# Optimization experiments

Hardware: AMD Instinct MI355X
Metric: run time of the kernel (lower is better)

The kernel has to match this reference:

```python
import jax, jax.numpy as jnp
import numpy as np

EPS_MSG = 1e-7   # GENConv message epsilon
BN_EPS = 1e-5    # BatchNorm1d eps
NUM_GRAPHS = 1024


def _linear(x, W, b):
    return x @ W + b


def _batchnorm(x, gamma, beta):
    # training-mode batch statistics over the node dimension
    mu = jnp.mean(x, axis=0)
    var = jnp.mean((x - mu) ** 2, axis=0)
    return (x - mu) * jax.lax.rsqrt(var + BN_EPS) * gamma + beta


def _genconv(x, src, dst, e, t, W1, b1, gamma, beta, W2, b2, num_nodes):
    # message: relu(x_j + edge_attr) + eps, shape [E, H]
    msg = jax.nn.relu(x[src] + e) + EPS_MSG
    # learnable softmax aggregation over each destination's neighborhood
    s = msg * t
    m = jax.lax.stop_gradient(jax.ops.segment_max(s, dst, num_segments=num_nodes))
    m = jnp.where(jnp.isfinite(m), m, 0.0)
    ex = jnp.exp(s - m[dst])
    denom = jax.ops.segment_sum(ex, dst, num_segments=num_nodes)
    alpha = ex / (denom[dst] + 1e-16)
    agg = jax.ops.segment_sum(msg * alpha, dst, num_segments=num_nodes)  # [N, H]
    # GENConv MLP([H, 2H, H], norm='batch') applied to x + aggregated messages
    h = x + agg
    h = _linear(h, W1, b1)
    h = _batchnorm(h, gamma, beta)
    h = jax.nn.relu(h)
    return _linear(h, W2, b2)


def setup_inputs() -> dict:
    key = jax.random.key(0)
    N, E, FIN, FE, H, L, G, OUT = 50000, 1000000, 32, 16, 64, 4, NUM_GRAPHS, 1
    ks = jax.random.split(key, 32)

    def rn(k, shape, fan_in):
        return jax.random.normal(k, shape, dtype=jnp.float32) * (1.0 / np.sqrt(fan_in))

    inp = {}
    inp["x"] = jax.random.normal(ks[0], (N, FIN), dtype=jnp.float32)
    inp["edge_attr"] = jax.random.normal(ks[1], (E, FE), dtype=jnp.float32)
    inp["edge_index"] = jax.random.randint(ks[2], (2, E), 0, N)
    inp["batch"] = jnp.sort(jax.random.randint(ks[3], (N,), 0, G))
    # atom encoder: Linear(FIN,H) ReLU Linear(H,H) ReLU
    inp["atom_W1"] = rn(ks[4], (FIN, H), FIN); inp["atom_b1"] = jnp.zeros((H,), jnp.float32)
    inp["atom_W2"] = rn(ks[5], (H, H), H);     inp["atom_b2"] = jnp.zeros((H,), jnp.float32)
    # bond encoder: Linear(FE,H) ReLU Linear(H,H) ReLU
    inp["bond_W1"] = rn(ks[6], (FE, H), FE);   inp["bond_b1"] = jnp.zeros((H,), jnp.float32)
    inp["bond_W2"] = rn(ks[7], (H, H), H);     inp["bond_b2"] = jnp.zeros((H,), jnp.float32)
    # stacked GENConv params (L layers)
    inp["conv_t"] = jnp.ones((L,), jnp.float32)
    inp["conv_W1"] = rn(ks[8], (L, H, 2 * H), H)
    inp["conv_b1"] = jnp.zeros((L, 2 * H), jnp.float32)
    inp["conv_gamma"] = jnp.ones((L, 2 * H), jnp.float32)
    inp["conv_beta"] = jnp.zeros((L, 2 * H), jnp.float32)
    inp["conv_W2"] = rn(ks[9], (L, 2 * H, H), 2 * H)
    inp["conv_b2"] = jnp.zeros((L, H), jnp.float32)
    # head
    inp["lin1_W"] = rn(ks[10], (H, H), H);     inp["lin1_b"] = jnp.zeros((H,), jnp.float32)
    inp["lin2_W"] = rn(ks[11], (H, OUT), H);   inp["lin2_b"] = jnp.zeros((OUT,), jnp.float32)
    return inp


def reference(x, edge_attr, atom_W1, atom_b1, atom_W2, atom_b2,
              bond_W1, bond_b1, bond_W2, bond_b2,
              conv_t, conv_W1, conv_b1, conv_gamma, conv_beta, conv_W2, conv_b2,
              lin1_W, lin1_b, lin2_W, lin2_b,
              edge_index, batch):
    N = x.shape[0]
    src, dst = edge_index[0], edge_index[1]
    h = jax.nn.relu(_linear(jax.nn.relu(_linear(x, atom_W1, atom_b1)), atom_W2, atom_b2))
    e = jax.nn.relu(_linear(jax.nn.relu(_linear(edge_attr, bond_W1, bond_b1)), bond_W2, bond_b2))
    L = conv_t.shape[0]
    for i in range(L):
        h = _genconv(h, src, dst, e, conv_t[i], conv_W1[i], conv_b1[i],
                     conv_gamma[i], conv_beta[i], conv_W2[i], conv_b2[i], N)
        if i < L - 1:
            h = jax.nn.relu(h)
    g = jax.ops.segment_sum(h, batch, num_segments=NUM_GRAPHS)  # global_add_pool
    g = jax.nn.relu(_linear(g, lin1_W, lin1_b))
    return _linear(g, lin2_W, lin2_b)
```

## Files before the change

kernel.cpp:

```cpp
#include <hip/hip_runtime.h>
#include <hip/hip_bf16.h>
#include <math.h>

typedef __attribute__((ext_vector_type(8))) short bf16x8;
typedef __attribute__((ext_vector_type(4))) float f32x4;

__device__ inline unsigned f2bf(float f) {
    union { __hip_bfloat16 h; unsigned short u; } cv;
    cv.h = __float2bfloat16(f);
    return (unsigned)cv.u;
}
__device__ inline float bfu(unsigned u) {
    return __uint_as_float(u << 16);
}


__global__ void k_hist(const int* __restrict__ dst, int* __restrict__ counts, int E) {
    int e = blockIdx.x * blockDim.x + threadIdx.x;
    if (e < E) atomicAdd(&counts[dst[e]], 1);
}

__global__ void k_scan1(const int* __restrict__ counts, int* __restrict__ row_ptr,
                        int* __restrict__ csum, int n) {
    __shared__ int buf[1024];
    int tid = threadIdx.x;
    int base = blockIdx.x * 1024;
    int v = (base + tid < n) ? counts[base + tid] : 0;
    buf[tid] = v;
    __syncthreads();
    int inc = v;
    for (int off = 1; off < 1024; off <<= 1) {
        int add = (tid >= off) ? buf[tid - off] : 0;
        __syncthreads();
        inc += add;
        buf[tid] = inc;
        __syncthreads();
    }
    if (base + tid < n) row_ptr[base + tid] = inc - v;
    if (tid == 1023) csum[blockIdx.x] = inc;
}

__global__ void k_scan2(int* __restrict__ csum, int nc, int* __restrict__ total) {
    if (threadIdx.x == 0) {
        int run = 0;
        for (int i = 0; i < nc; ++i) { int c = csum[i]; csum[i] = run; run += c; }
        *total = run;
    }
}

__global__ void k_scan3(int* __restrict__ row_ptr, const int* __restrict__ csum,
                        const int* __restrict__ total, int n) {
    int i = blockIdx.x * blockDim.x + threadIdx.x;
    if (i < n) row_ptr[i] += csum[i >> 10];
    if (i == 0) row_ptr[n] = *total;
}

#define ECH 4096
__global__ __launch_bounds__(256) void k_scatter(const int* __restrict__ src,
                          const int* __restrict__ dst,
                          const int* __restrict__ row_ptr, int* __restrict__ fill,
                          int2* __restrict__ spe, int E, int NS) {
    int bs = blockIdx.x & 7;
    int chunk = blockIdx.x >> 3;
    int base = chunk * ECH;
    int lo = bs * NS, hi = lo + NS;
#pragma unroll 1
    for (int j = 0; j < ECH / 256; ++j) {
        int e = base + j * 256 + threadIdx.x;
        if (e < E) {
            int d = dst[e];
            if (d >= lo && d < hi) {
                int pos = row_ptr[d] + atomicAdd(&fill[d], 1);
                spe[pos] = make_int2(src[e], e);
            }
        }
    }
}

__global__ void k_gptr(const int* __restrict__ batch, int* __restrict__ gptr, int n, int G) {
    int i = blockIdx.x * blockDim.x + threadIdx.x;
    if (i > n) return;
    if (i == 0) {
        int b0 = batch[0];
        for (int g = 0; g <= b0; ++g) gptr[g] = 0;
    } else if (i == n) {
        int bl = batch[n - 1];
        for (int g = bl + 1; g <= G; ++g) gptr[g] = n;
    } else {
        int b = batch[i], pb = batch[i - 1];
        for (int g = pb + 1; g <= b; ++g) gptr[g] = i;
    }
}


__global__ void k_wt(const float* __restrict__ W1, const float* __restrict__ W2,
                     unsigned short* __restrict__ W1b, unsigned short* __restrict__ W2tb) {
    int tid = blockIdx.x * blockDim.x + threadIdx.x;
    if (tid < 1024) {
        int j = tid / 16, k = tid % 16;
        W1b[j * 16 + k] = (unsigned short)f2bf(W1[k * 64 + j]);
    }
    if (tid < 4096) {
        int j = tid / 64, k = tid % 64;
        W2tb[j * 64 + k] = (unsigned short)f2bf(W2[k * 64 + j]);
    }
}


#define TM 128
__global__ __launch_bounds__(256) void k_atom(const float* __restrict__ x,
        const float* __restrict__ W1, const float* __restrict__ b1,
        const float* __restrict__ W2, const float* __restrict__ b2,
        float* __restrict__ out, unsigned short* __restrict__ hb, int M) {
    __shared__ float sU[TM * 65];
    __shared__ float sW1[32 * 64];
    __shared__ float sW2[64 * 64];
    __shared__ float sB1[64], sB2[64];
#define A_IN(r, c) sU[(r) * 33 + (c)]
#define A_T1(r, c) sU[(r) * 65 + (c)]
    int tid = threadIdx.x;
    int base = blockIdx.x * TM;
    for (int i = tid; i < 32 * 64 / 4; i += 256) ((float4*)sW1)[i] = ((const float4*)W1)[i];
    for (int i = tid; i < 64 * 64 / 4; i += 256) ((float4*)sW2)[i] = ((const float4*)W2)[i];
    if (tid < 64) { sB1[tid] = b1[tid]; sB2[tid] = b2[tid]; }
    for (int i = tid; i < TM * 32 / 4; i += 256) {
        int r = i / 8, c4 = i % 8;
        int row = base + r;
        float4 v = (row < M) ? ((const float4*)(x + (long)row * 32))[c4] : make_float4(0, 0, 0, 0);
        A_IN(r, c4 * 4 + 0) = v.x; A_IN(r, c4 * 4 + 1) = v.y;
        A_IN(r, c4 * 4 + 2) = v.z; A_IN(r, c4 * 4 + 3) = v.w;
    }
    __syncthreads();
    int r0 = (tid / 16) * 8;
    int c0 = (tid % 16) * 4;
    float acc[8][4];
#pragma unroll
    for (int i = 0; i < 8; i++)
#pragma unroll
        for (int j = 0; j < 4; j++) acc[i][j] = sB1[c0 + j];
    for (int k = 0; k < 32; k++) {
        float a[8], b[4];
#pragma unroll
        for (int i = 0; i < 8; i++) a[i] = A_IN(r0 + i, k);
#pragma unroll
        for (int j = 0; j < 4; j++) b[j] = sW1[k * 64 + c0 + j];
#pragma unroll
        for (int i = 0; i < 8; i++)
#pragma unroll
            for (int j = 0; j < 4; j++) acc[i][j] += a[i] * b[j];
    }
    __syncthreads();
#pragma unroll
    for (int i = 0; i < 8; i++)
#pragma unroll
        for (int j = 0; j < 4; j++) A_T1(r0 + i, c0 + j) = fmaxf(acc[i][j], 0.f);
    __syncthreads();
#pragma unroll
    for (int i = 0; i < 8; i++)
#pragma unroll
        for (int j = 0; j < 4; j++) acc[i][j] = sB2[c0 + j];
    for (int k = 0; k < 64; k++) {
        float a[8], b[4];
#pragma unroll
        for (int i = 0; i < 8; i++) a[i] = A_T1(r0 + i, k);
#pragma unroll
        for (int j = 0; j < 4; j++) b[j] = sW2[k * 64 + c0 + j];
#pragma unroll
        for (int i = 0; i < 8; i++)
#pragma unroll
            for (int j = 0; j < 4; j++) acc[i][j] += a[i] * b[j];
    }
#pragma unroll
    for (int i = 0; i < 8; i++) {
        int row = base + r0 + i;
        if (row < M) {
            float4 v = make_float4(fmaxf(acc[i][0], 0.f), fmaxf(acc[i][1], 0.f),
                                   fmaxf(acc[i][2], 0.f), fmaxf(acc[i][3], 0.f));
            *(float4*)(out + (long)row * 64 + c0) = v;
            unsigned p01 = f2bf(v.x) | (f2bf(v.y) << 16);
            unsigned p23 = f2bf(v.z) | (f2bf(v.w) << 16);
            *(uint2*)(hb + (long)row * 64 + c0) = make_uint2(p01, p23);
        }
    }
}


__global__ __launch_bounds__(256) void k_bond(const float* __restrict__ ea,
        const int2* __restrict__ spe,
        const unsigned short* __restrict__ W1b, const float* __restrict__ b1,
        const unsigned short* __restrict__ W2tb, const float* __restrict__ b2,
        unsigned short* __restrict__ e_q, int E) {
    __shared__ unsigned sT1[128 * 32];
    __shared__ unsigned sW2[64 * 32];
    int tid = threadIdx.x;

    for (int i = tid; i < 2048; i += 256) {
        int rw = i >> 5, cp = i & 31;
        sW2[rw * 32 + (cp ^ ((rw & 7) << 2))] = ((const unsigned*)W2tb)[i];
    }

    int wv = tid >> 6, lane = tid & 63;
    int lr = lane & 15, q = lane >> 4;

    union { bf16x8 v; uint4 u4; } bf1[4];
    float bias1[4];
#pragma unroll
    for (int nt = 0; nt < 4; ++nt) {
        bf1[nt].u4 = make_uint4(0, 0, 0, 0);
        if (q < 2)
            bf1[nt].u4 = *(const uint4*)(W1b + (nt * 16 + lr) * 16 + q * 8);
        bias1[nt] = b1[nt * 16 + lr];
    }

#pragma unroll
    for (int mt1 = 0; mt1 < 2; ++mt1) {
        int rtile = wv * 2 + mt1;
        long row1 = (long)blockIdx.x * 128 + rtile * 16 + lr;
        long eidx = row1 < (long)E ? row1 : (long)(E - 1);
        int eid = spe[eidx].y;
        union { bf16x8 v; uint4 u4; unsigned u[4]; } af1;
        af1.u4 = make_uint4(0, 0, 0, 0);
        if (q < 2) {
            const float4* er = (const float4*)(ea + (long)eid * 16 + q * 8);
            float4 u0 = er[0], u1 = er[1];
            af1.u[0] = f2bf(u0.x) | (f2bf(u0.y) << 16);
            af1.u[1] = f2bf(u0.z) | (f2bf(u0.w) << 16);
            af1.u[2] = f2bf(u1.x) | (f2bf(u1.y) << 16);
            af1.u[3] = f2bf(u1.z) | (f2bf(u1.w) << 16);
        }
#pragma unroll
        for (int nt = 0; nt < 4; ++nt) {
            f32x4 c0;
            c0[0] = bias1[nt]; c0[1] = bias1[nt]; c0[2] = bias1[nt]; c0[3] = bias1[nt];
            f32x4 d = __builtin_amdgcn_mfma_f32_16x16x32_bf16(af1.v, bf1[nt].v, c0, 0, 0, 0);
#pragma unroll
            for (int i = 0; i < 4; ++i) {
                unsigned hv = f2bf(fmaxf(d[i], 0.f));
                unsigned ov = (unsigned)__shfl_xor((int)hv, 1, 64);
                if ((lr & 1) == 0) {
                    int r = rtile * 16 + q * 4 + i;
                    int cp = nt * 8 + (lr >> 1);
                    sT1[r * 32 + (cp ^ ((r & 7) << 2))] = hv | (ov << 16);
                }
            }
        }
    }
    __syncthreads();

    bf16x8 bf[4][2];
#pragma unroll
    for (int nt = 0; nt < 4; ++nt)
#pragma unroll
        for (int ks = 0; ks < 2; ++ks) {
            int rw = nt * 16 + lr;
            int u = rw * 32 + ((ks * 16 + q * 4) ^ ((rw & 7) << 2));
            bf[nt][ks] = *(const bf16x8*)&sW2[u];
        }
    f32x4 acc[2][4];
#pragma unroll
    for (int mt = 0; mt < 2; ++mt)
#pragma unroll
        for (int nt = 0; nt < 4; ++nt) {
            float bias = b2[nt * 16 + lr];
            f32x4 c0; c0[0] = bias; c0[1] = bias; c0[2] = bias; c0[3] = bias;
            acc[mt][nt] = c0;
        }
#pragma unroll
    for (int mt = 0; mt < 2; ++mt) {
        int rw = (wv * 2 + mt) * 16 + lr;
#pragma unroll
        for (int ks = 0; ks < 2; ++ks) {
            int u = rw * 32 + ((ks * 16 + q * 4) ^ ((rw & 7) << 2));
            bf16x8 af = *(const bf16x8*)&sT1[u];
#pragma unroll
            for (int nt = 0; nt < 4; ++nt)
                acc[mt][nt] = __builtin_amdgcn_mfma_f32_16x16x32_bf16(
                    af, bf[nt][ks], acc[mt][nt], 0, 0, 0);
        }
    }
#pragma unroll
    for (int mt = 0; mt < 2; ++mt)
#pragma unroll
        for (int nt = 0; nt < 4; ++nt) {
            long r0 = (long)blockIdx.x * 128 + (wv * 2 + mt) * 16 + q * 4;
            unsigned p01 = f2bf(fmaxf(acc[mt][nt][0], 0.f)) |
                           (f2bf(fmaxf(acc[mt][nt][1], 0.f)) << 16);
            unsigned p23 = f2bf(fmaxf(acc[mt][nt][2], 0.f)) |
                           (f2bf(fmaxf(acc[mt][nt][3], 0.f)) << 16);
            long qb = ((r0 >> 2) * 64 + nt * 16 + lr) * 4;
            if (r0 + 3 < (long)E) {
                *(uint2*)(e_q + qb) = make_uint2(p01, p23);
            } else {
                unsigned vv[4] = {p01 & 0xffff, p01 >> 16, p23 & 0xffff, p23 >> 16};
#pragma unroll
                for (int i = 0; i < 4; ++i)
                    if (r0 + i < (long)E) e_q[qb + i] = (unsigned short)vv[i];
            }
        }
}


__global__ __launch_bounds__(256) void k_agg(const float* __restrict__ h,
        const unsigned short* __restrict__ h_bf,
        const unsigned short* __restrict__ e_q, const int2* __restrict__ spe,
        const int* __restrict__ row_ptr, const float* __restrict__ t_ptr, int layer,
        float* __restrict__ y, int n) {
    int wid = blockIdx.x * 4 + (threadIdx.x >> 6);
    int lane = threadIdx.x & 63;
    if (wid >= n) return;
    wid = __builtin_amdgcn_readfirstlane(wid);
    float tval = t_ptr[layer];
    int beg = row_ptr[wid], end = row_ptr[wid + 1];
    float m = -INFINITY, den = 0.f, num = 0.f;
    int i = beg;
    int astart = (beg + 3) & ~3; if (astart > end) astart = end;
    int aend = end & ~3;         if (aend < astart) aend = astart;
    for (; i < astart; ++i) {
        int s = spe[i].x;
        float ev = bfu((unsigned)e_q[((long)(i >> 2) * 64 + lane) * 4 + (i & 3)]);
        float hv = bfu((unsigned)h_bf[(long)s * 64 + lane]);
        float msg = fmaxf(hv + ev, 0.f) + 1e-7f;
        float sv = msg * tval;
        float mn = fmaxf(m, sv);
        float sc = __expf(m - mn);
        float w = __expf(sv - mn);
        den = den * sc + w;
        num = num * sc + w * msg;
        m = mn;
    }
    for (; i + 8 <= aend; i += 8) {
        int s0 = spe[i].x,     s1 = spe[i + 1].x, s2 = spe[i + 2].x, s3 = spe[i + 3].x;
        int s4 = spe[i + 4].x, s5 = spe[i + 5].x, s6 = spe[i + 6].x, s7 = spe[i + 7].x;
        uint2 ea0 = *(const uint2*)(e_q + ((long)(i >> 2) * 64 + lane) * 4);
        uint2 ea1 = *(const uint2*)(e_q + ((long)((i >> 2) + 1) * 64 + lane) * 4);
        float hv0 = bfu((unsigned)h_bf[(long)s0 * 64 + lane]);
        float hv1 = bfu((unsigned)h_bf[(long)s1 * 64 + lane]);
        float hv2 = bfu((unsigned)h_bf[(long)s2 * 64 + lane]);
        float hv3 = bfu((unsigned)h_bf[(long)s3 * 64 + lane]);
        float hv4 = bfu((unsigned)h_bf[(long)s4 * 64 + lane]);
        float hv5 = bfu((unsigned)h_bf[(long)s5 * 64 + lane]);
        float hv6 = bfu((unsigned)h_bf[(long)s6 * 64 + lane]);
        float hv7 = bfu((unsigned)h_bf[(long)s7 * 64 + lane]);
        float msg0 = fmaxf(hv0 + bfu(ea0.x & 0xffff), 0.f) + 1e-7f;
        float msg1 = fmaxf(hv1 + bfu(ea0.x >> 16), 0.f) + 1e-7f;
        float msg2 = fmaxf(hv2 + bfu(ea0.y & 0xffff), 0.f) + 1e-7f;
        float msg3 = fmaxf(hv3 + bfu(ea0.y >> 16), 0.f) + 1e-7f;
        float msg4 = fmaxf(hv4 + bfu(ea1.x & 0xffff), 0.f) + 1e-7f;
        float msg5 = fmaxf(hv5 + bfu(ea1.x >> 16), 0.f) + 1e-7f;
        float msg6 = fmaxf(hv6 + bfu(ea1.y & 0xffff), 0.f) + 1e-7f;
        float msg7 = fmaxf(hv7 + bfu(ea1.y >> 16), 0.f) + 1e-7f;
        float sv0 = msg0 * tval, sv1 = msg1 * tval, sv2 = msg2 * tval, sv3 = msg3 * tval;
        float sv4 = msg4 * tval, sv5 = msg5 * tval, sv6 = msg6 * tval, sv7 = msg7 * tval;
        float mn = fmaxf(fmaxf(fmaxf(fmaxf(m, sv0), fmaxf(sv1, sv2)),
                               fmaxf(fmaxf(sv3, sv4), fmaxf(sv5, sv6))), sv7);
        float sc = __expf(m - mn);
        float w0 = __expf(sv0 - mn), w1 = __expf(sv1 - mn);
        float w2 = __expf(sv2 - mn), w3 = __expf(sv3 - mn);
        float w4 = __expf(sv4 - mn), w5 = __expf(sv5 - mn);
        float w6 = __expf(sv6 - mn), w7 = __expf(sv7 - mn);
        den = den * sc + (((w0 + w1) + (w2 + w3)) + ((w4 + w5) + (w6 + w7)));
        num = num * sc + (((w0 * msg0 + w1 * msg1) + (w2 * msg2 + w3 * msg3)) +
                          ((w4 * msg4 + w5 * msg5) + (w6 * msg6 + w7 * msg7)));
        m = mn;
    }
    for (; i < aend; i += 4) {
        int s0 = spe[i].x, s1 = spe[i + 1].x, s2 = spe[i + 2].x, s3 = spe[i + 3].x;
        uint2 ee = *(const uint2*)(e_q + ((long)(i >> 2) * 64 + lane) * 4);
        float hv0 = bfu((unsigned)h_bf[(long)s0 * 64 + lane]);
        float hv1 = bfu((unsigned)h_bf[(long)s1 * 64 + lane]);
        float hv2 = bfu((unsigned)h_bf[(long)s2 * 64 + lane]);
        float hv3 = bfu((unsigned)h_bf[(long)s3 * 64 + lane]);
        float msg0 = fmaxf(hv0 + bfu(ee.x & 0xffff), 0.f) + 1e-7f;
        float msg1 = fmaxf(hv1 + bfu(ee.x >> 16), 0.f) + 1e-7f;
        float msg2 = fmaxf(hv2 + bfu(ee.y & 0xffff), 0.f) + 1e-7f;
        float msg3 = fmaxf(hv3 + bfu(ee.y >> 16), 0.f) + 1e-7f;
        float sv0 = msg0 * tval, sv1 = msg1 * tval;
        float sv2 = msg2 * tval, sv3 = msg3 * tval;
        float mn = fmaxf(fmaxf(fmaxf(m, sv0), fmaxf(sv1, sv2)), sv3);
        float sc = __expf(m - mn);
        float w0 = __expf(sv0 - mn);
        float w1 = __expf(sv1 - mn);
        float w2 = __expf(sv2 - mn);
        float w3 = __expf(sv3 - mn);
        den = den * sc + ((w0 + w1) + (w2 + w3));
        num = num * sc + ((w0 * msg0 + w1 * msg1) + (w2 * msg2 + w3 * msg3));
        m = mn;
    }
    for (; i < end; ++i) {
        int s = spe[i].x;
        float ev = bfu((unsigned)e_q[((long)(i >> 2) * 64 + lane) * 4 + (i & 3)]);
        float hv = bfu((unsigned)h_bf[(long)s * 64 + lane]);
        float msg = fmaxf(hv + ev, 0.f) + 1e-7f;
        float sv = msg * tval;
        float mn = fmaxf(m, sv);
        float sc = __expf(m - mn);
        float w = __expf(sv - mn);
        den = den * sc + w;
        num = num * sc + w * msg;
        m = mn;
    }
    float agg = (end > beg) ? num / (den + 1e-16f) : 0.f;
    y[(long)wid * 64 + lane] = h[(long)wid * 64 + lane] + agg;
}


__global__ __launch_bounds__(256) void k_gemm1(const float* __restrict__ y,
        const float* __restrict__ W1, const float* __restrict__ b1,
        float* __restrict__ h1, float* __restrict__ part, int n) {
    __shared__ float sA[64][65];
    __shared__ float sW[64 * 128];
    __shared__ float sB[128];
    __shared__ float sS[8][128];
    __shared__ float sS2[8][128];
    int tid = threadIdx.x;
    int base = blockIdx.x * 64;
    for (int i = tid; i < 64 * 128 / 4; i += 256) ((float4*)sW)[i] = ((const float4*)W1)[i];
    if (tid < 128) sB[tid] = b1[tid];
    for (int i = tid; i < 64 * 64 / 4; i += 256) {
        int r = i / 16, c4 = i % 16;
        int row = base + r;
        float4 v = (row < n) ? ((const float4*)(y + (long)row * 64))[c4] : make_float4(0, 0, 0, 0);
        sA[r][c4 * 4 + 0] = v.x; sA[r][c4 * 4 + 1] = v.y;
        sA[r][c4 * 4 + 2] = v.z; sA[r][c4 * 4 + 3] = v.w;
    }
    __syncthreads();
    int rg = tid / 32;
    int r0 = rg * 8;
    int c0 = (tid % 32) * 4;
    float acc[8][4];
#pragma unroll
    for (int i = 0; i < 8; i++)
#pragma unroll
        for (int j = 0; j < 4; j++) acc[i][j] = sB[c0 + j];
    for (int k = 0; k < 64; k++) {
        float a[8], b[4];
#pragma unroll
        for (int i = 0; i < 8; i++) a[i] = sA[r0 + i][k];
#pragma unroll
        for (int j = 0; j < 4; j++) b[j] = sW[k * 128 + c0 + j];
#pragma unroll
        for (int i = 0; i < 8; i++)
#pragma unroll
            for (int j = 0; j < 4; j++) acc[i][j] += a[i] * b[j];
    }
    float ps[4] = {0, 0, 0, 0}, ps2[4] = {0, 0, 0, 0};
#pragma unroll
    for (int i = 0; i < 8; i++) {
        int row = base + r0 + i;
        if (row < n) {
            float4 v = make_float4(acc[i][0], acc[i][1], acc[i][2], acc[i][3]);
            *(float4*)(h1 + (long)row * 128 + c0) = v;
#pragma unroll
            for (int j = 0; j < 4; j++) { ps[j] += acc[i][j]; ps2[j] += acc[i][j] * acc[i][j]; }
        }
    }
#pragma unroll
    for (int j = 0; j < 4; j++) { sS[rg][c0 + j] = ps[j]; sS2[rg][c0 + j] = ps2[j]; }
    __syncthreads();
    if (tid < 128) {
        float s = 0.f, s2 = 0.f;
#pragma unroll
        for (int g = 0; g < 8; g++) { s += sS[g][tid]; s2 += sS2[g][tid]; }
        part[blockIdx.x * 256 + tid] = s;
        part[blockIdx.x * 256 + 128 + tid] = s2;
    }
}


__global__ __launch_bounds__(256) void k_bnred(const float* __restrict__ part,
                                               float* __restrict__ part2, int nblk) {
    int c = threadIdx.x;
    int b = blockIdx.x;
    float s = 0.f;
    for (int r = b; r < nblk; r += 64) s += part[r * 256 + c];
    part2[b * 256 + c] = s;
}

__global__ __launch_bounds__(1024) void k_bnfin(const float* __restrict__ part2,
                        const float* __restrict__ gamma, const float* __restrict__ beta,
                        float* __restrict__ scale, float* __restrict__ shift, float invN) {
    __shared__ float red[4][256];
    __shared__ float tot[256];
    int c = threadIdx.x & 255;
    int g = threadIdx.x >> 8;
    float s = 0.f;
#pragma unroll
    for (int r = 0; r < 16; ++r) s += part2[(g * 16 + r) * 256 + c];
    red[g][c] = s;
    __syncthreads();
    if (threadIdx.x < 256) tot[c] = red[0][c] + red[1][c] + red[2][c] + red[3][c];
    __syncthreads();
    if (threadIdx.x < 128) {
        int cc = threadIdx.x;
        float mu = tot[cc] * invN;
        float var = fmaxf(tot[128 + cc] * invN - mu * mu, 0.f);
        float sc = gamma[cc] * rsqrtf(var + 1e-5f);
        scale[cc] = sc;
        shift[cc] = beta[cc] - mu * sc;
    }
}


__global__ __launch_bounds__(256) void k_gemm2(const float* __restrict__ h1,
        const float* __restrict__ scale, const float* __restrict__ shift,
        const float* __restrict__ W2, const float* __restrict__ b2,
        float* __restrict__ hout, unsigned short* __restrict__ hb, int n, int dorelu) {
    __shared__ float sA[32][129];
    __shared__ float sW[128 * 64];
    __shared__ float sSc[128], sSh[128], sB[64];
    int tid = threadIdx.x;
    int base = blockIdx.x * 32;
    for (int i = tid; i < 128 * 64 / 4; i += 256) ((float4*)sW)[i] = ((const float4*)W2)[i];
    if (tid < 128) { sSc[tid] = scale[tid]; sSh[tid] = shift[tid]; }
    if (tid < 64) sB[tid] = b2[tid];
    __syncthreads();
    for (int i = tid; i < 32 * 128 / 4; i += 256) {
        int r = i / 32, c4 = i % 32;
        int row = base + r;
        float4 v = (row < n) ? ((const float4*)(h1 + (long)row * 128))[c4] : make_float4(0, 0, 0, 0);
        int c = c4 * 4;
        sA[r][c + 0] = fmaxf(v.x * sSc[c + 0] + sSh[c + 0], 0.f);
        sA[r][c + 1] = fmaxf(v.y * sSc[c + 1] + sSh[c + 1], 0.f);
        sA[r][c + 2] = fmaxf(v.z * sSc[c + 2] + sSh[c + 2], 0.f);
        sA[r][c + 3] = fmaxf(v.w * sSc[c + 3] + sSh[c + 3], 0.f);
    }
    __syncthreads();
    int r0 = (tid / 16) * 2;
    int c0 = (tid % 16) * 4;
    float acc[2][4];
#pragma unroll
    for (int i = 0; i < 2; i++)
#pragma unroll
        for (int j = 0; j < 4; j++) acc[i][j] = sB[c0 + j];
    for (int k = 0; k < 128; k++) {
        float a[2], b[4];
#pragma unroll
        for (int i = 0; i < 2; i++) a[i] = sA[r0 + i][k];
#pragma unroll
        for (int j = 0; j < 4; j++) b[j] = sW[k * 64 + c0 + j];
#pragma unroll
        for (int i = 0; i < 2; i++)
#pragma unroll
            for (int j = 0; j < 4; j++) acc[i][j] += a[i] * b[j];
    }
#pragma unroll
    for (int i = 0; i < 2; i++) {
        int row = base + r0 + i;
        if (row < n) {
            float4 v;
            v.x = dorelu ? fmaxf(acc[i][0], 0.f) : acc[i][0];
            v.y = dorelu ? fmaxf(acc[i][1], 0.f) : acc[i][1];
            v.z = dorelu ? fmaxf(acc[i][2], 0.f) : acc[i][2];
            v.w = dorelu ? fmaxf(acc[i][3], 0.f) : acc[i][3];
            *(float4*)(hout + (long)row * 64 + c0) = v;
            if (dorelu) {
                unsigned p01 = f2bf(v.x) | (f2bf(v.y) << 16);
                unsigned p23 = f2bf(v.z) | (f2bf(v.w) << 16);
                *(uint2*)(hb + (long)row * 64 + c0) = make_uint2(p01, p23);
            }
        }
    }
}


__global__ __launch_bounds__(64) void k_head(const float* __restrict__ h,
        const int* __restrict__ gptr,
        const float* __restrict__ W1, const float* __restrict__ b1,
        const float* __restrict__ W2, const float* __restrict__ b2,
        float* __restrict__ out) {
    int g = blockIdx.x;
    int lane = threadIdx.x;
    int beg = gptr[g], end = gptr[g + 1];
    float s = 0.f;
    for (int r = beg; r < end; ++r) s += h[(long)r * 64 + lane];
    __shared__ float sg[64];
    sg[lane] = s;
    __syncthreads();
    float acc = b1[lane];
    for (int k = 0; k < 64; k++) acc += sg[k] * W1[k * 64 + lane];
    acc = fmaxf(acc, 0.f);
    float v = acc * W2[lane];
#pragma unroll
    for (int off = 32; off > 0; off >>= 1) v += __shfl_down(v, off, 64);
    if (lane == 0) out[g] = v + b2[0];
}


extern "C" void kernel_launch(void* const* d_in, const int* in_sizes, int n_in,
                              void* d_out, int out_size, void* d_ws, size_t ws_size,
                              hipStream_t stream) {
    const float* x      = (const float*)d_in[0];
    const float* ea     = (const float*)d_in[1];
    const int*   ei     = (const int*)d_in[2];
    const int*   batch  = (const int*)d_in[3];
    const float* atomW1 = (const float*)d_in[4];
    const float* atomb1 = (const float*)d_in[5];
    const float* atomW2 = (const float*)d_in[6];
    const float* atomb2 = (const float*)d_in[7];
    const float* bondW1 = (const float*)d_in[8];
    const float* bondb1 = (const float*)d_in[9];
    const float* bondW2 = (const float*)d_in[10];
    const float* bondb2 = (const float*)d_in[11];
    const float* convT  = (const float*)d_in[12];
    const float* convW1 = (const float*)d_in[13];
    const float* convb1 = (const float*)d_in[14];
    const float* convG  = (const float*)d_in[15];
    const float* convBt = (const float*)d_in[16];
    const float* convW2 = (const float*)d_in[17];
    const float* convb2 = (const float*)d_in[18];
    const float* lin1W  = (const float*)d_in[19];
    const float* lin1b  = (const float*)d_in[20];
    const float* lin2W  = (const float*)d_in[21];
    const float* lin2b  = (const float*)d_in[22];
    float* out = (float*)d_out;

    const int N = in_sizes[0] / 32;
    const int E = in_sizes[1] / 16;
    const int G = out_size;
    const int Lconv = in_sizes[12];
    const int nchunk = (N + 1023) / 1024;
    const int nblk1 = (N + 63) / 64;
    const int NS = (N + 7) / 8;
    const int nchE = (E + ECH - 1) / ECH;
    const size_t nquad = (size_t)((E + 3) / 4);

    size_t need = 0;
    auto count = [&](size_t bytes) { need += (bytes + 255) & ~(size_t)255; };
    count(nquad * 4 * 64 * 2);
    count((size_t)N * 64 * 4);
    count((size_t)N * 64 * 2);
    count((size_t)N * 64 * 4);
    count((size_t)N * 128 * 4);
    count((size_t)E * 8);
    count((size_t)(N + 1) * 4);
    count((size_t)N * 4);
    count((size_t)N * 4);
    count((size_t)(G + 1) * 4);
    count((size_t)nblk1 * 256 * 4);
    count((size_t)64 * 256 * 4);
    count(128 * 4); count(128 * 4);
    count((size_t)(nchunk + 1) * 4);
    count(4);
    count(1024 * 2);
    count(4096 * 2);
    if (ws_size < need) {
        hipMemsetAsync(d_out, 0, (size_t)out_size * 4, stream);
        return;
    }

    char* ws = (char*)d_ws;
    size_t off = 0;
    auto alloc = [&](size_t bytes) -> void* {
        void* p = ws + off;
        off += (bytes + 255) & ~(size_t)255;
        return p;
    };
    unsigned short* e_q = (unsigned short*)alloc(nquad * 4 * 64 * 2);
    float* h_cur    = (float*)alloc((size_t)N * 64 * 4);
    unsigned short* h_bf = (unsigned short*)alloc((size_t)N * 64 * 2);
    float* y_buf    = (float*)alloc((size_t)N * 64 * 4);
    float* h1       = (float*)alloc((size_t)N * 128 * 4);
    int2*  spe      = (int2*)alloc((size_t)E * 8);
    int*   row_ptr  = (int*)alloc((size_t)(N + 1) * 4);
    int*   counts   = (int*)alloc((size_t)N * 4);
    int*   fill     = (int*)alloc((size_t)N * 4);
    int*   gptr     = (int*)alloc((size_t)(G + 1) * 4);
    float* part     = (float*)alloc((size_t)nblk1 * 256 * 4);
    float* part2    = (float*)alloc((size_t)64 * 256 * 4);
    float* bnscale  = (float*)alloc(128 * 4);
    float* bnshift  = (float*)alloc(128 * 4);
    int*   csum     = (int*)alloc((size_t)(nchunk + 1) * 4);
    int*   totalp   = (int*)alloc(4);
    unsigned short* W1b  = (unsigned short*)alloc(1024 * 2);
    unsigned short* W2tb = (unsigned short*)alloc(4096 * 2);
    (void)n_in;

    hipMemsetAsync(counts, 0, (size_t)N * 4, stream);
    hipMemsetAsync(fill, 0, (size_t)N * 4, stream);

    const int* src = ei;
    const int* dst = ei + E;

    k_hist<<<(E + 255) / 256, 256, 0, stream>>>(dst, counts, E);
    k_scan1<<<nchunk, 1024, 0, stream>>>(counts, row_ptr, csum, N);
    k_scan2<<<1, 64, 0, stream>>>(csum, nchunk, totalp);
    k_scan3<<<(N + 255) / 256, 256, 0, stream>>>(row_ptr, csum, totalp, N);
    k_scatter<<<nchE * 8, 256, 0, stream>>>(src, dst, row_ptr, fill, spe, E, NS);
    k_gptr<<<(N + 256) / 256, 256, 0, stream>>>(batch, gptr, N, G);
    k_wt<<<16, 256, 0, stream>>>(bondW1, bondW2, W1b, W2tb);

    k_atom<<<(N + TM - 1) / TM, 256, 0, stream>>>(x, atomW1, atomb1, atomW2, atomb2,
                                                  h_cur, h_bf, N);
    k_bond<<<(E + 127) / 128, 256, 0, stream>>>(ea, spe, W1b, bondb1, W2tb, bondb2, e_q, E);

    for (int l = 0; l < Lconv; ++l) {
        k_agg<<<(N + 3) / 4, 256, 0, stream>>>(h_cur, h_bf, e_q, spe, row_ptr, convT, l,
                                               y_buf, N);
        k_gemm1<<<nblk1, 256, 0, stream>>>(y_buf, convW1 + (size_t)l * 64 * 128,
                                           convb1 + (size_t)l * 128, h1, part, N);
        k_bnred<<<64, 256, 0, stream>>>(part, part2, nblk1);
        k_bnfin<<<1, 1024, 0, stream>>>(part2, convG + (size_t)l * 128, convBt + (size_t)l * 128,
                                        bnscale, bnshift, 1.0f / (float)N);
        k_gemm2<<<(N + 31) / 32, 256, 0, stream>>>(h1, bnscale, bnshift,
                                                   convW2 + (size_t)l * 128 * 64,
                                                   convb2 + (size_t)l * 64, h_cur, h_bf, N,
                                                   (l < Lconv - 1) ? 1 : 0);
    }

    k_head<<<G, 64, 0, stream>>>(h_cur, gptr, lin1W, lin1b, lin2W, lin2b, out);
}
```

Before: 611.2 us.

## Move GENConv MLP GEMMs to bf16 MFMA with bf16 intermediate buffers

Rewrites both per-layer MLP GEMM kernels to use bf16 16x16x32 MFMA instructions with swizzled LDS tiles, instead of scalar fp32 FMA loops. The aggregation output and the hidden activations between the two GEMMs are now stored in bf16, which halves their memory traffic. Conv weights are pre-transposed to bf16 once by a new kernel. This cuts ALU and memory cost of the GEMM stages at the price of bf16 rounding in the batchnorm input and the MLP path.

```diff
diff --git a/kernel.cpp b/kernel.cpp
--- a/kernel.cpp
+++ b/kernel.cpp
@@ -103,6 +103,21 @@
     if (tid < 4096) {
         int j = tid / 64, k = tid % 64;
         W2tb[j * 64 + k] = (unsigned short)f2bf(W2[k * 64 + j]);
+    }
+}
+
+__global__ void k_wtc(const float* __restrict__ W1, const float* __restrict__ W2,
+                      unsigned short* __restrict__ W1tb, unsigned short* __restrict__ W2tb,
+                      int L) {
+    int idx = blockIdx.x * blockDim.x + threadIdx.x;
+    int tot = L * 8192;
+    if (idx < tot) {
+        int l = idx / 8192, r = idx % 8192;
+        int j = r / 64, k = r % 64;
+        W1tb[(long)l * 8192 + j * 64 + k] = (unsigned short)f2bf(W1[(long)l * 8192 + k * 128 + j]);
+        int j2 = r / 128, k2 = r % 128;
+        W2tb[(long)l * 8192 + j2 * 128 + k2] =
+            (unsigned short)f2bf(W2[(long)l * 8192 + k2 * 64 + j2]);
     }
 }
 
@@ -304,7 +319,7 @@
         const unsigned short* __restrict__ h_bf,
         const unsigned short* __restrict__ e_q, const int2* __restrict__ spe,
         const int* __restrict__ row_ptr, const float* __restrict__ t_ptr, int layer,
-        float* __restrict__ y, int n) {
+        unsigned short* __restrict__ yb, int n) {
     int wid = blockIdx.x * 4 + (threadIdx.x >> 6);
     int lane = threadIdx.x & 63;
     if (wid >= n) return;
@@ -400,69 +415,77 @@
         m = mn;
     }
     float agg = (end > beg) ? num / (den + 1e-16f) : 0.f;
-    y[(long)wid * 64 + lane] = h[(long)wid * 64 + lane] + agg;
-}
-
-
-__global__ __launch_bounds__(256) void k_gemm1(const float* __restrict__ y,
-        const float* __restrict__ W1, const float* __restrict__ b1,
-        float* __restrict__ h1, float* __restrict__ part, int n) {
-    __shared__ float sA[64][65];
-    __shared__ float sW[64 * 128];
-    __shared__ float sB[128];
-    __shared__ float sS[8][128];
-    __shared__ float sS2[8][128];
+    yb[(long)wid * 64 + lane] = (unsigned short)f2bf(h[(long)wid * 64 + lane] + agg);
+}
+
+
+__global__ __launch_bounds__(256) void k_gemm1(const unsigned* __restrict__ yb,
+        const unsigned* __restrict__ W1tb, const float* __restrict__ b1,
+        unsigned* __restrict__ h1b, float* __restrict__ part, int n) {
+    __shared__ unsigned sY[128 * 32];
+    __shared__ unsigned sW[128 * 32];
     int tid = threadIdx.x;
-    int base = blockIdx.x * 64;
-    for (int i = tid; i < 64 * 128 / 4; i += 256) ((float4*)sW)[i] = ((const float4*)W1)[i];
-    if (tid < 128) sB[tid] = b1[tid];
-    for (int i = tid; i < 64 * 64 / 4; i += 256) {
-        int r = i / 16, c4 = i % 16;
-        int row = base + r;
-        float4 v = (row < n) ? ((const float4*)(y + (long)row * 64))[c4] : make_float4(0, 0, 0, 0);
-        sA[r][c4 * 4 + 0] = v.x; sA[r][c4 * 4 + 1] = v.y;
-        sA[r][c4 * 4 + 2] = v.z; sA[r][c4 * 4 + 3] = v.w;
-    }
-    __syncthreads();
-    int rg = tid / 32;
-    int r0 = rg * 8;
-    int c0 = (tid % 32) * 4;
-    float acc[8][4];
-#pragma unroll
-    for (int i = 0; i < 8; i++)
-#pragma unroll
-        for (int j = 0; j < 4; j++) acc[i][j] = sB[c0 + j];
-    for (int k = 0; k < 64; k++) {
-        float a[8], b[4];
-#pragma unroll
-        for (int i = 0; i < 8; i++) a[i] = sA[r0 + i][k];
-#pragma unroll
-        for (int j = 0; j < 4; j++) b[j] = sW[k * 128 + c0 + j];
-#pragma unroll
-        for (int i = 0; i < 8; i++)
-#pragma unroll
-            for (int j = 0; j < 4; j++) acc[i][j] += a[i] * b[j];
-    }
-    float ps[4] = {0, 0, 0, 0}, ps2[4] = {0, 0, 0, 0};
-#pragma unroll
-    for (int i = 0; i < 8; i++) {
-        int row = base + r0 + i;
-        if (row < n) {
-            float4 v = make_float4(acc[i][0], acc[i][1], acc[i][2], acc[i][3]);
-            *(float4*)(h1 + (long)row * 128 + c0) = v;
-#pragma unroll
-            for (int j = 0; j < 4; j++) { ps[j] += acc[i][j]; ps2[j] += acc[i][j] * acc[i][j]; }
-        }
-    }
-#pragma unroll
-    for (int j = 0; j < 4; j++) { sS[rg][c0 + j] = ps[j]; sS2[rg][c0 + j] = ps2[j]; }
-    __syncthreads();
-    if (tid < 128) {
-        float s = 0.f, s2 = 0.f;
-#pragma unroll
-        for (int g = 0; g < 8; g++) { s += sS[g][tid]; s2 += sS2[g][tid]; }
-        part[blockIdx.x * 256 + tid] = s;
-        part[blockIdx.x * 256 + 128 + tid] = s2;
+    int base = blockIdx.x * 128;
+    for (int i = tid; i < 4096; i += 256) {
+        int rw = i >> 5, cp = i & 31;
+        sW[rw * 32 + (cp ^ ((rw & 7) << 2))] = W1tb[i];
+    }
+#pragma unroll
+    for (int j = 0; j < 16; ++j) {
+        int u = j * 256 + tid;
+        int r = u >> 5, cp = u & 31;
+        long row = base + r;
+        unsigned v = (row < (long)n) ? yb[row * 32 + cp] : 0u;
+        sY[r * 32 + (cp ^ ((r & 7) << 2))] = v;
+    }
+    __syncthreads();
+    int wv = tid >> 6, lane = tid & 63, lr = lane & 15, q = lane >> 4;
+    bf16x8 bf[2][2];
+    float bias[2];
+#pragma unroll
+    for (int nt2 = 0; nt2 < 2; ++nt2) {
+        int rw = wv * 32 + nt2 * 16 + lr;
+#pragma unroll
+        for (int ks = 0; ks < 2; ++ks)
+            bf[nt2][ks] = *(const bf16x8*)&sW[rw * 32 + ((ks * 16 + q * 4) ^ ((rw & 7) << 2))];
+        bias[nt2] = b1[rw];
+    }
+    float ps[2] = {0, 0}, ps2[2] = {0, 0};
+#pragma unroll 1
+    for (int mt = 0; mt < 8; ++mt) {
+        int ar = mt * 16 + lr;
+        bf16x8 a0 = *(const bf16x8*)&sY[ar * 32 + ((q * 4) ^ ((ar & 7) << 2))];
+        bf16x8 a1 = *(const bf16x8*)&sY[ar * 32 + ((16 + q * 4) ^ ((ar & 7) << 2))];
+#pragma unroll
+        for (int nt2 = 0; nt2 < 2; ++nt2) {
+            f32x4 acc;
+            acc[0] = bias[nt2]; acc[1] = bias[nt2]; acc[2] = bias[nt2]; acc[3] = bias[nt2];
+            acc = __builtin_amdgcn_mfma_f32_16x16x32_bf16(a0, bf[nt2][0], acc, 0, 0, 0);
+            acc = __builtin_amdgcn_mfma_f32_16x16x32_bf16(a1, bf[nt2][1], acc, 0, 0, 0);
+            int col = wv * 32 + nt2 * 16 + lr;
+#pragma unroll
+            for (int i = 0; i < 4; ++i) {
+                long row = base + mt * 16 + q * 4 + i;
+                float v = acc[i];
+                unsigned hv = f2bf(v);
+                unsigned ov = (unsigned)__shfl_xor((int)hv, 1, 64);
+                bool in = row < (long)n;
+                if (in) { ps[nt2] += v; ps2[nt2] += v * v; }
+                if (in && (lr & 1) == 0)
+                    h1b[row * 64 + ((unsigned)col >> 1)] = hv | (ov << 16);
+            }
+        }
+    }
+#pragma unroll
+    for (int nt2 = 0; nt2 < 2; ++nt2) {
+        float s = ps[nt2], s2 = ps2[nt2];
+        s += __shfl_down(s, 32, 64);  s += __shfl_down(s, 16, 64);
+        s2 += __shfl_down(s2, 32, 64); s2 += __shfl_down(s2, 16, 64);
+        if (lane < 16) {
+            int col = wv * 32 + nt2 * 16 + lr;
+            part[(long)blockIdx.x * 256 + col] = s;
+            part[(long)blockIdx.x * 256 + 128 + col] = s2;
+        }
     }
 }
 
@@ -472,7 +495,7 @@
     int c = threadIdx.x;
     int b = blockIdx.x;
     float s = 0.f;
-    for (int r = b; r < nblk; r += 64) s += part[r * 256 + c];
+    for (int r = b; r < nblk; r += 64) s += part[(long)r * 256 + c];
     part2[b * 256 + c] = s;
 }
 
@@ -501,62 +524,66 @@
 }
 
 
-__global__ __launch_bounds__(256) void k_gemm2(const float* __restrict__ h1,
+__global__ __launch_bounds__(256) void k_gemm2(const unsigned* __restrict__ h1b,
         const float* __restrict__ scale, const float* __restrict__ shift,
-        const float* __restrict__ W2, const float* __restrict__ b2,
+        const unsigned* __restrict__ W2tbL, const float* __restrict__ b2,
         float* __restrict__ hout, unsigned short* __restrict__ hb, int n, int dorelu) {
-    __shared__ float sA[32][129];
-    __shared__ float sW[128 * 64];
-    __shared__ float sSc[128], sSh[128], sB[64];
+    __shared__ unsigned sA[128 * 64];
+    __shared__ unsigned sW[64 * 64];
+    __shared__ float sSc[128], sSh[128];
     int tid = threadIdx.x;
-    int base = blockIdx.x * 32;
-    for (int i = tid; i < 128 * 64 / 4; i += 256) ((float4*)sW)[i] = ((const float4*)W2)[i];
+    int base = blockIdx.x * 128;
     if (tid < 128) { sSc[tid] = scale[tid]; sSh[tid] = shift[tid]; }
-    if (tid < 64) sB[tid] = b2[tid];
-    __syncthreads();
-    for (int i = tid; i < 32 * 128 / 4; i += 256) {
-        int r = i / 32, c4 = i % 32;
-        int row = base + r;
-        float4 v = (row < n) ? ((const float4*)(h1 + (long)row * 128))[c4] : make_float4(0, 0, 0, 0);
-        int c = c4 * 4;
-        sA[r][c + 0] = fmaxf(v.x * sSc[c + 0] + sSh[c + 0], 0.f);
-        sA[r][c + 1] = fmaxf(v.y * sSc[c + 1] + sSh[c + 1], 0.f);
-        sA[r][c + 2] = fmaxf(v.z * sSc[c + 2] + sSh[c + 2], 0.f);
-        sA[r][c + 3] = fmaxf(v.w * sSc[c + 3] + sSh[c + 3], 0.f);
-    }
-    __syncthreads();
-    int r0 = (tid / 16) * 2;
-    int c0 = (tid % 16) * 4;
-    float acc[2][4];
-#pragma unroll
-    for (int i = 0; i < 2; i++)
-#pragma unroll
-        for (int j = 0; j < 4; j++) acc[i][j] = sB[c0 + j];
-    for (int k = 0; k < 128; k++) {
-        float a[2], b[4];
-#pragma unroll
-        for (int i = 0; i < 2; i++) a[i] = sA[r0 + i][k];
-#pragma unroll
-        for (int j = 0; j < 4; j++) b[j] = sW[k * 64 + c0 + j];
-#pragma unroll
-        for (int i = 0; i < 2; i++)
-#pragma unroll
-            for (int j = 0; j < 4; j++) acc[i][j] += a[i] * b[j];
-    }
-#pragma unroll
-    for (int i = 0; i < 2; i++) {
-        int row = base + r0 + i;
-        if (row < n) {
-            float4 v;
-            v.x = dorelu ? fmaxf(acc[i][0], 0.f) : acc[i][0];
-            v.y = dorelu ? fmaxf(acc[i][1], 0.f) : acc[i][1];
-            v.z = dorelu ? fmaxf(acc[i][2], 0.f) : acc[i][2];
-            v.w = dorelu ? fmaxf(acc[i][3], 0.f) : acc[i][3];
-            *(float4*)(hout + (long)row * 64 + c0) = v;
-            if (dorelu) {
-                unsigned p01 = f2bf(v.x) | (f2bf(v.y) << 16);
-                unsigned p23 = f2bf(v.z) | (f2bf(v.w) << 16);
-                *(uint2*)(hb + (long)row * 64 + c0) = make_uint2(p01, p23);
+    for (int i = tid; i < 4096; i += 256) {
+        int rw = i >> 6, cp = i & 63;
+        sW[rw * 64 + (cp ^ ((rw & 7) << 2))] = W2tbL[i];
+    }
+    __syncthreads();
+#pragma unroll
+    for (int j = 0; j < 32; ++j) {
+        int u = j * 256 + tid;
+        int r = u >> 6, cp = u & 63;
+        long row = base + r;
+        unsigned w = 0;
+        if (row < (long)n) {
+            unsigned hv = h1b[row * 64 + cp];
+            float v0 = fmaxf(bfu(hv & 0xffff) * sSc[2 * cp] + sSh[2 * cp], 0.f);
+            float v1 = fmaxf(bfu(hv >> 16) * sSc[2 * cp + 1] + sSh[2 * cp + 1], 0.f);
+            w = f2bf(v0) | (f2bf(v1) << 16);
+        }
+        sA[r * 64 + (cp ^ ((r & 7) << 2))] = w;
+    }
+    __syncthreads();
+    int wv = tid >> 6, lane = tid & 63, lr = lane & 15, q = lane >> 4;
+    bf16x8 bf[4];
+    {
+        int rw = wv * 16 + lr;
+#pragma unroll
+        for (int ks = 0; ks < 4; ++ks)
+            bf[ks] = *(const bf16x8*)&sW[rw * 64 + ((ks * 16 + q * 4) ^ ((rw & 7) << 2))];
+    }
+    float bias = b2[wv * 16 + lr];
+#pragma unroll 1
+    for (int mt = 0; mt < 8; ++mt) {
+        int ar = mt * 16 + lr;
+        f32x4 acc;
+        acc[0] = bias; acc[1] = bias; acc[2] = bias; acc[3] = bias;
+#pragma unroll
+        for (int ks = 0; ks < 4; ++ks) {
+            bf16x8 a = *(const bf16x8*)&sA[ar * 64 + ((ks * 16 + q * 4) ^ ((ar & 7) << 2))];
+            acc = __builtin_amdgcn_mfma_f32_16x16x32_bf16(a, bf[ks], acc, 0, 0, 0);
+        }
+        int col = wv * 16 + lr;
+#pragma unroll
+        for (int i = 0; i < 4; ++i) {
+            long row = base + mt * 16 + q * 4 + i;
+            float v = dorelu ? fmaxf(acc[i], 0.f) : acc[i];
+            unsigned hv = f2bf(v);
+            unsigned ov = (unsigned)__shfl_xor((int)hv, 1, 64);
+            if (row < (long)n) {
+                hout[row * 64 + col] = v;
+                if (dorelu && (lr & 1) == 0)
+                    *(unsigned*)(hb + row * 64 + (col & ~1)) = hv | (ov << 16);
             }
         }
     }
@@ -619,7 +646,7 @@
     const int G = out_size;
     const int Lconv = in_sizes[12];
     const int nchunk = (N + 1023) / 1024;
-    const int nblk1 = (N + 63) / 64;
+    const int nblk128 = (N + 127) / 128;
     const int NS = (N + 7) / 8;
     const int nchE = (E + ECH - 1) / ECH;
     const size_t nquad = (size_t)((E + 3) / 4);
@@ -629,20 +656,22 @@
     count(nquad * 4 * 64 * 2);
     count((size_t)N * 64 * 4);
     count((size_t)N * 64 * 2);
-    count((size_t)N * 64 * 4);
-    count((size_t)N * 128 * 4);
+    count((size_t)N * 64 * 2);
+    count((size_t)N * 128 * 2);
     count((size_t)E * 8);
     count((size_t)(N + 1) * 4);
     count((size_t)N * 4);
     count((size_t)N * 4);
     count((size_t)(G + 1) * 4);
-    count((size_t)nblk1 * 256 * 4);
+    count((size_t)nblk128 * 256 * 4);
     count((size_t)64 * 256 * 4);
     count(128 * 4); count(128 * 4);
     count((size_t)(nchunk + 1) * 4);
     count(4);
     count(1024 * 2);
     count(4096 * 2);
+    count((size_t)Lconv * 8192 * 2);
+    count((size_t)Lconv * 8192 * 2);
     if (ws_size < need) {
         hipMemsetAsync(d_out, 0, (size_t)out_size * 4, stream);
         return;
@@ -658,14 +687,14 @@
     unsigned short* e_q = (unsigned short*)alloc(nquad * 4 * 64 * 2);
     float* h_cur    = (float*)alloc((size_t)N * 64 * 4);
     unsigned short* h_bf = (unsigned short*)alloc((size_t)N * 64 * 2);
-    float* y_buf    = (float*)alloc((size_t)N * 64 * 4);
-    float* h1       = (float*)alloc((size_t)N * 128 * 4);
+    unsigned short* y_bf = (unsigned short*)alloc((size_t)N * 64 * 2);
+    unsigned short* h1b  = (unsigned short*)alloc((size_t)N * 128 * 2);
     int2*  spe      = (int2*)alloc((size_t)E * 8);
     int*   row_ptr  = (int*)alloc((size_t)(N + 1) * 4);
     int*   counts   = (int*)alloc((size_t)N * 4);
     int*   fill     = (int*)alloc((size_t)N * 4);
     int*   gptr     = (int*)alloc((size_t)(G + 1) * 4);
-    float* part     = (float*)alloc((size_t)nblk1 * 256 * 4);
+    float* part     = (float*)alloc((size_t)nblk128 * 256 * 4);
     float* part2    = (float*)alloc((size_t)64 * 256 * 4);
     float* bnscale  = (float*)alloc(128 * 4);
     float* bnshift  = (float*)alloc(128 * 4);
@@ -673,6 +702,8 @@
     int*   totalp   = (int*)alloc(4);
     unsigned short* W1b  = (unsigned short*)alloc(1024 * 2);
     unsigned short* W2tb = (unsigned short*)alloc(4096 * 2);
+    unsigned short* cW1tb = (unsigned short*)alloc((size_t)Lconv * 8192 * 2);
+    unsigned short* cW2tb = (unsigned short*)alloc((size_t)Lconv * 8192 * 2);
     (void)n_in;
 
     hipMemsetAsync(counts, 0, (size_t)N * 4, stream);
@@ -688,6 +719,7 @@
     k_scatter<<<nchE * 8, 256, 0, stream>>>(src, dst, row_ptr, fill, spe, E, NS);
     k_gptr<<<(N + 256) / 256, 256, 0, stream>>>(batch, gptr, N, G);
     k_wt<<<16, 256, 0, stream>>>(bondW1, bondW2, W1b, W2tb);
+    k_wtc<<<(Lconv * 8192 + 255) / 256, 256, 0, stream>>>(convW1, convW2, cW1tb, cW2tb, Lconv);
 
     k_atom<<<(N + TM - 1) / TM, 256, 0, stream>>>(x, atomW1, atomb1, atomW2, atomb2,
                                                   h_cur, h_bf, N);
@@ -695,16 +727,18 @@
 
     for (int l = 0; l < Lconv; ++l) {
         k_agg<<<(N + 3) / 4, 256, 0, stream>>>(h_cur, h_bf, e_q, spe, row_ptr, convT, l,
-                                               y_buf, N);
-        k_gemm1<<<nblk1, 256, 0, stream>>>(y_buf, convW1 + (size_t)l * 64 * 128,
-                                           convb1 + (size_t)l * 128, h1, part, N);
-        k_bnred<<<64, 256, 0, stream>>>(part, part2, nblk1);
+                                               y_bf, N);
+        k_gemm1<<<nblk128, 256, 0, stream>>>((const unsigned*)y_bf,
+                                             (const unsigned*)(cW1tb + (size_t)l * 8192),
+                                             convb1 + (size_t)l * 128,
+                                             (unsigned*)h1b, part, N);
+        k_bnred<<<64, 256, 0, stream>>>(part, part2, nblk128);
         k_bnfin<<<1, 1024, 0, stream>>>(part2, convG + (size_t)l * 128, convBt + (size_t)l * 128,
                                         bnscale, bnshift, 1.0f / (float)N);
-        k_gemm2<<<(N + 31) / 32, 256, 0, stream>>>(h1, bnscale, bnshift,
-                                                   convW2 + (size_t)l * 128 * 64,
-                                                   convb2 + (size_t)l * 64, h_cur, h_bf, N,
-                                                   (l < Lconv - 1) ? 1 : 0);
+        k_gemm2<<<nblk128, 256, 0, stream>>>((const unsigned*)h1b, bnscale, bnshift,
+                                             (const unsigned*)(cW2tb + (size_t)l * 8192),
+                                             convb2 + (size_t)l * 64, h_cur, h_bf, N,
+                                             (l < Lconv - 1) ? 1 : 0);
     }
 
     k_head<<<G, 64, 0, stream>>>(h_cur, gptr, lin1W, lin1b, lin2W, lin2b, out);
```

Measured after the change: 535.1 us. 1.14x faster.
